# Optimization experiments

Hardware: AMD Instinct MI355X
Metric: run time of the kernel (lower is better)

The kernel has to match this reference:

```python
import jax, jax.numpy as jnp
import numpy as np

D_INPUT = 2048
DD_DIM = 512
DD_PAIRS = DD_DIM // 2


def setup_inputs() -> dict:
    key = jax.random.key(0)
    k1, k2, k3 = jax.random.split(key, 3)
    x = jax.random.normal(k1, (4, 4096, D_INPUT), dtype=jnp.float32)
    # Learned projection (zeros at init in torch; use small random for a non-trivial test)
    W = jax.random.normal(k2, (DD_PAIRS, D_INPUT), dtype=jnp.float32) * 0.02
    b = jax.random.normal(k3, (DD_PAIRS,), dtype=jnp.float32) * 0.02
    return {"x": x, "W": W, "b": b}


def reference(x, W, b):
    # x: (B, T, D); W: (P, D); b: (P,) with P = DD_DIM // 2
    deltas = jnp.einsum('btd,pd->btp', x, W) + b          # (B, T, P)
    angles = jnp.cumsum(deltas, axis=1)                   # cumulative phase
    cos, sin = jnp.cos(angles), jnp.sin(angles)
    x1 = x[..., :DD_PAIRS]                                # (B, T, P)
    x2 = x[..., DD_PAIRS:DD_DIM]                          # (B, T, P)
    rotated = jnp.concatenate([x1 * cos - x2 * sin, x2 * cos + x1 * sin], axis=-1)
    return jnp.concatenate([rotated, x[..., DD_DIM:]], axis=-1)
```

## Files before the change

### kernel.cpp

```cpp
#include <hip/hip_runtime.h>
#include <math.h>

#define BB 4
#define TT 4096
#define DDIM 2048
#define PP 256
#define MM (BB*TT)
#define KKDIM 2048
#define CHUNK 32
#define NCHUNK (TT/CHUNK)

#define BK 32
#define KSTEPS (KKDIM/BK)
#define LROW 72

typedef __attribute__((ext_vector_type(8))) short short8;
typedef __attribute__((ext_vector_type(4))) float f32x4;

__device__ __forceinline__ unsigned short f2bf(float f) {
    unsigned u = __float_as_uint(f);
    u += 0x7FFF + ((u >> 16) & 1);
    return (unsigned short)(u >> 16);
}
__device__ __forceinline__ float bf2f(unsigned short h) {
    return __uint_as_float(((unsigned)h) << 16);
}

__device__ __forceinline__ void cvt8(const float4& va, const float4& vb,
                                     short8& hi, short8& lo) {
    float f[8] = {va.x, va.y, va.z, va.w, vb.x, vb.y, vb.z, vb.w};
    #pragma unroll
    for (int j = 0; j < 8; ++j) {
        unsigned short h = f2bf(f[j]);
        hi[j] = (short)h;
        lo[j] = (short)f2bf(f[j] - bf2f(h));
    }
}

__device__ __forceinline__ void cvt4(const float4& v, uint2& hp, uint2& lp) {
    unsigned short h0 = f2bf(v.x), h1 = f2bf(v.y), h2 = f2bf(v.z), h3 = f2bf(v.w);
    unsigned short l0 = f2bf(v.x - bf2f(h0)), l1 = f2bf(v.y - bf2f(h1));
    unsigned short l2 = f2bf(v.z - bf2f(h2)), l3 = f2bf(v.w - bf2f(h3));
    hp.x = (unsigned)h0 | ((unsigned)h1 << 16); hp.y = (unsigned)h2 | ((unsigned)h3 << 16);
    lp.x = (unsigned)l0 | ((unsigned)l1 << 16); lp.y = (unsigned)l2 | ((unsigned)l3 << 16);
}

__global__ __launch_bounds__(256) void prep_wf_k(const float* __restrict__ W,
                                                 unsigned short* __restrict__ Wfh,
                                                 unsigned short* __restrict__ Wfl) {
    const int f = blockIdx.x * 256 + threadIdx.x;
    const int lane = f & 63;
    const int nb   = (f >> 6) & 15;
    const int k0i  = f >> 10;
    const int row  = nb * 16 + (lane & 15);
    const int kk   = k0i * 32 + (lane >> 4) * 8;
    const float* src = W + (size_t)row * KKDIM + kk;
    float4 a = *(const float4*)src;
    float4 b = *(const float4*)(src + 4);
    short8 hi, lo;
    cvt8(a, b, hi, lo);
    *(short8*)(Wfh + (size_t)f * 8) = hi;
    *(short8*)(Wfl + (size_t)f * 8) = lo;
}

#define GSTEP(CUR, NXT, BHc, BLc, BHn, BLn, IT)                               \
{                                                                             \
    const bool last_ = ((IT) == KSTEPS - 1);                                  \
    const int  kA_   = last_ ? (IT) * BK : ((IT) + 1) * BK;                   \
    float4 av0_ = *(const float4*)(xs0 + kA_);                                \
    float4 av1_ = *(const float4*)(xs1 + kA_);                                \
    const int k0iN_ = last_ ? (IT) : (IT) + 1;                                \
    _Pragma("unroll")                                                         \
    for (int nt = 0; nt < 2; ++nt) {                                          \
        size_t o = bfbase + (size_t)(k0iN_ * 16 + nt) * 512;                  \
        BHn[nt] = *(const short8*)(Wfh + o);                                  \
        BLn[nt] = *(const short8*)(Wfl + o);                                  \
    }                                                                         \
    short8 ah_[2], al_[2];                                                    \
    _Pragma("unroll")                                                         \
    for (int mt = 0; mt < 2; ++mt) {                                          \
        int idx = (wm * 32 + mt * 16 + lm) * LROW + ko * 8;                   \
        ah_[mt] = *(const short8*)&Ast[CUR][idx];                             \
        al_[mt] = *(const short8*)&Ast[CUR][idx + 32];                        \
    }                                                                         \
    _Pragma("unroll")                                                         \
    for (int mt = 0; mt < 2; ++mt)                                            \
        _Pragma("unroll")                                                     \
        for (int nt = 0; nt < 2; ++nt) {                                      \
            f32x4 c = acc[mt][nt];                                            \
            c = __builtin_amdgcn_mfma_f32_16x16x32_bf16(ah_[mt], BHc[nt], c, 0, 0, 0); \
            c = __builtin_amdgcn_mfma_f32_16x16x32_bf16(ah_[mt], BLc[nt], c, 0, 0, 0); \
            c = __builtin_amdgcn_mfma_f32_16x16x32_bf16(al_[mt], BHc[nt], c, 0, 0, 0); \
            acc[mt][nt] = c;                                                  \
        }                                                                     \
    uint2 hp0_, lp0_, hp1_, lp1_;                                             \
    cvt4(av0_, hp0_, lp0_);                                                   \
    cvt4(av1_, hp1_, lp1_);                                                   \
    *(uint2*)&Ast[NXT][sidx0]      = hp0_;                                    \
    *(uint2*)&Ast[NXT][sidx0 + 32] = lp0_;                                    \
    *(uint2*)&Ast[NXT][sidx1]      = hp1_;                                    \
    *(uint2*)&Ast[NXT][sidx1 + 32] = lp1_;                                    \
    if (docopy && !last_ && kA_ >= 512) {                                     \
        *(float4*)(os0 + kA_) = av0_;                                         \
        *(float4*)(os1 + kA_) = av1_;                                         \
    }                                                                         \
    __syncthreads();                                                          \
}

__global__ __launch_bounds__(512, 4) void gemm4_k(const float* __restrict__ x,
                                                  const unsigned short* __restrict__ Wfh,
                                                  const unsigned short* __restrict__ Wfl,
                                                  const float* __restrict__ bias,
                                                  float* __restrict__ delta,
                                                  float* __restrict__ csum,
                                                  float* __restrict__ out) {
    __shared__ unsigned short Ast[2][128 * LROW];

    const int hw      = blockIdx.y * 4 + blockIdx.x;
    const int logical = (hw & 7) * 64 + (hw >> 3);
    const int nidx    = logical & 3;
    const int midx    = logical >> 2;
    const int n0      = nidx * 64;
    const int m0      = midx * 128;
    const bool docopy = (nidx == 0);

    const int tid  = threadIdx.x;
    const int w    = tid >> 6;
    const int wm   = w >> 1;
    const int wn   = w & 1;
    const int lane = tid & 63;
    const int lm   = lane & 15;
    const int ko   = lane >> 4;

    const int arow0 = tid >> 3;
    const int ach   = tid & 7;
    const int sidx0 = arow0 * LROW + ach * 4;
    const int sidx1 = (64 + arow0) * LROW + ach * 4;
    const float* xs0 = x + (size_t)(m0 + arow0) * KKDIM + ach * 4;
    const float* xs1 = x + (size_t)(m0 + 64 + arow0) * KKDIM + ach * 4;
    float* os0 = out + (size_t)(m0 + arow0) * DDIM + ach * 4;
    float* os1 = out + (size_t)(m0 + 64 + arow0) * DDIM + ach * 4;

    const size_t bfbase = ((size_t)(nidx * 4 + wn * 2) * 64 + (size_t)lane) * 8;

    f32x4 acc[2][2];
    #pragma unroll
    for (int i = 0; i < 2; ++i)
        #pragma unroll
        for (int j = 0; j < 2; ++j) {
            f32x4 z = {0.f, 0.f, 0.f, 0.f};
            acc[i][j] = z;
        }

    short8 bhA[2], blA[2], bhB[2], blB[2];

    {
        float4 a0 = *(const float4*)(xs0);
        float4 a1 = *(const float4*)(xs1);
        uint2 hp, lp;
        cvt4(a0, hp, lp);
        *(uint2*)&Ast[0][sidx0]      = hp;
        *(uint2*)&Ast[0][sidx0 + 32] = lp;
        cvt4(a1, hp, lp);
        *(uint2*)&Ast[0][sidx1]      = hp;
        *(uint2*)&Ast[0][sidx1 + 32] = lp;
        #pragma unroll
        for (int nt = 0; nt < 2; ++nt) {
            size_t o = bfbase + (size_t)nt * 512;
            bhA[nt] = *(const short8*)(Wfh + o);
            blA[nt] = *(const short8*)(Wfl + o);
        }
        __syncthreads();
    }

    for (int it = 0; it < KSTEPS; it += 2) {
        GSTEP(0, 1, bhA, blA, bhB, blB, it)
        GSTEP(1, 0, bhB, blB, bhA, blA, it + 1)
    }

    float bsv[2];
    #pragma unroll
    for (int nt = 0; nt < 2; ++nt) bsv[nt] = bias[n0 + wn * 32 + nt * 16 + lm];

    float cs[2] = {0.f, 0.f};
    #pragma unroll
    for (int mt = 0; mt < 2; ++mt)
        #pragma unroll
        for (int nt = 0; nt < 2; ++nt)
            #pragma unroll
            for (int r = 0; r < 4; ++r) {
                float val = acc[mt][nt][r] + bsv[nt];
                int m = m0 + wm * 32 + mt * 16 + ko * 4 + r;
                delta[(size_t)m * PP + n0 + wn * 32 + nt * 16 + lm] = val;
                cs[nt] += val;
            }
    #pragma unroll
    for (int nt = 0; nt < 2; ++nt) {
        float s = cs[nt];
        s += __shfl_xor(s, 16);
        s += __shfl_xor(s, 32);
        if (lane < 16)
            csum[(size_t)(m0 / CHUNK + wm) * PP + n0 + wn * 32 + nt * 16 + lane] = s;
    }
}

__global__ __launch_bounds__(256) void rotate4_k(const float* __restrict__ delta,
                                                 const float* __restrict__ csum,
                                                 const float* __restrict__ x,
                                                 float* __restrict__ out) {
    const int blk = blockIdx.x;
    const int seg = blk & 3;
    const int bc  = blk >> 2;
    const int c   = bc & (NCHUNK - 1);
    const int b   = bc >> 7;
    const int p   = threadIdx.x;

    const float* cs = csum + (size_t)(b * NCHUNK) * PP + p;
    float angle = 0.f;
    int c0 = 0;
    for (; c0 + 16 <= c; c0 += 16) {
        float v[16];
        #pragma unroll
        for (int j = 0; j < 16; ++j) v[j] = cs[(size_t)(c0 + j) * PP];
        #pragma unroll
        for (int j = 0; j < 16; ++j) angle += v[j];
    }
    for (; c0 < c; ++c0) angle += cs[(size_t)c0 * PP];

    const int tbase = bc * CHUNK;
    const float* dp = delta + (size_t)tbase * PP + p;

    const int tpre = seg * 8;
    for (int t = 0; t < tpre; t += 8) {
        float v[8];
        #pragma unroll
        for (int j = 0; j < 8; ++j) v[j] = dp[(size_t)(t + j) * PP];
        #pragma unroll
        for (int j = 0; j < 8; ++j) angle += v[j];
    }

    const float* xp = x + (size_t)tbase * DDIM + p;
    float*       op = out + (size_t)tbase * DDIM + p;
    const float inv2pi = 0.15915494309189535f;

    for (int t0 = tpre; t0 < tpre + 8; t0 += 4) {
        float dv[4], x1v[4], x2v[4];
        #pragma unroll
        for (int j = 0; j < 4; ++j) {
            dv[j]  = dp[(size_t)(t0 + j) * PP];
            x1v[j] = xp[(size_t)(t0 + j) * DDIM];
            x2v[j] = xp[(size_t)(t0 + j) * DDIM + PP];
        }
        #pragma unroll
        for (int j = 0; j < 4; ++j) {
            angle += dv[j];
            float r  = __builtin_amdgcn_fractf(angle * inv2pi);
            float s  = __builtin_amdgcn_sinf(r);
            float co = __builtin_amdgcn_cosf(r);
            op[(size_t)(t0 + j) * DDIM]      = x1v[j] * co - x2v[j] * s;
            op[(size_t)(t0 + j) * DDIM + PP] = x2v[j] * co + x1v[j] * s;
        }
    }
}

__global__ __launch_bounds__(256) void gemm_k(const float* __restrict__ x,
                                              const float* __restrict__ W,
                                              const float* __restrict__ bias,
                                              float* __restrict__ delta,
                                              int dstride, int doff) {
    __shared__ float As[16][68];
    __shared__ float Bs[16][68];
    const int m0  = blockIdx.x * 64;
    const int n0  = blockIdx.y * 64;
    const int tid = threadIdx.x;
    const int lr  = tid >> 2;
    const int lc  = (tid & 3) << 2;
    const int tmi = tid & 15;
    const int tni = tid >> 4;
    float acc[4][4] = {};
    for (int k0 = 0; k0 < KKDIM; k0 += 16) {
        float4 a4 = *(const float4*)(x + (size_t)(m0 + lr) * KKDIM + k0 + lc);
        float4 b4 = *(const float4*)(W + (size_t)(n0 + lr) * KKDIM + k0 + lc);
        __syncthreads();
        As[lc + 0][lr] = a4.x; As[lc + 1][lr] = a4.y;
        As[lc + 2][lr] = a4.z; As[lc + 3][lr] = a4.w;
        Bs[lc + 0][lr] = b4.x; Bs[lc + 1][lr] = b4.y;
        Bs[lc + 2][lr] = b4.z; Bs[lc + 3][lr] = b4.w;
        __syncthreads();
        #pragma unroll
        for (int kk = 0; kk < 16; ++kk) {
            float4 av = *(const float4*)&As[kk][tmi * 4];
            float4 bv = *(const float4*)&Bs[kk][tni * 4];
            float am[4] = {av.x, av.y, av.z, av.w};
            float bn[4] = {bv.x, bv.y, bv.z, bv.w};
            #pragma unroll
            for (int i = 0; i < 4; ++i)
                #pragma unroll
                for (int j = 0; j < 4; ++j)
                    acc[i][j] += am[i] * bn[j];
        }
    }
    const float4 b4 = *(const float4*)(bias + n0 + tni * 4);
    #pragma unroll
    for (int i = 0; i < 4; ++i) {
        size_t m = (size_t)(m0 + tmi * 4 + i);
        float4 o;
        o.x = acc[i][0] + b4.x; o.y = acc[i][1] + b4.y;
        o.z = acc[i][2] + b4.z; o.w = acc[i][3] + b4.w;
        *(float4*)(delta + m * dstride + doff + n0 + tni * 4) = o;
    }
}

__global__ __launch_bounds__(256) void chunksum_k(const float* __restrict__ delta,
                                                  int dstride, int doff,
                                                  float* __restrict__ csum, int cstride) {
    const int bc = blockIdx.x;
    const int b  = bc / NCHUNK;
    const int c  = bc % NCHUNK;
    const int p  = threadIdx.x;
    const int tbase = b * TT + c * CHUNK;
    float s = 0.f;
    #pragma unroll 8
    for (int t = 0; t < CHUNK; ++t)
        s += delta[(size_t)(tbase + t) * dstride + doff + p];
    csum[(size_t)bc * cstride + p] = s;
}

__global__ __launch_bounds__(256) void scan_k(float* __restrict__ csum, int cstride) {
    const int idx = blockIdx.x * 256 + threadIdx.x;
    const int b = idx >> 8;
    const int p = idx & 255;
    float run = 0.f;
    for (int c0 = 0; c0 < NCHUNK; c0 += 8) {
        float v[8];
        #pragma unroll
        for (int j = 0; j < 8; ++j)
            v[j] = csum[(size_t)(b * NCHUNK + c0 + j) * cstride + p];
        #pragma unroll
        for (int j = 0; j < 8; ++j) {
            float t = v[j];
            csum[(size_t)(b * NCHUNK + c0 + j) * cstride + p] = run;
            run += t;
        }
    }
}

__global__ __launch_bounds__(256) void rotate_k(const float* __restrict__ delta,
                                                int dstride, int doff,
                                                const float* __restrict__ csum, int cstride,
                                                const float* __restrict__ x,
                                                float* __restrict__ out) {
    const int bc = blockIdx.x;
    const int p  = threadIdx.x;
    const int tbase = bc * CHUNK;
    float angle = csum[(size_t)bc * cstride + p];
    for (int t = 0; t < CHUNK; ++t) {
        size_t row = (size_t)(tbase + t);
        angle += delta[row * dstride + doff + p];
        float s, co;
        sincosf(angle, &s, &co);
        float x1 = x[row * DDIM + p];
        float x2 = x[row * DDIM + PP + p];
        out[row * DDIM + p]      = x1 * co - x2 * s;
        out[row * DDIM + PP + p] = x2 * co + x1 * s;
    }
}

__global__ __launch_bounds__(256) void copy_k(const float* __restrict__ x,
                                              float* __restrict__ out) {
    const size_t row = (size_t)blockIdx.x * 4 + (threadIdx.x >> 6);
    const int lane = threadIdx.x & 63;
    const int col = 512 + (blockIdx.y * 64 + lane) * 4;
    const size_t a = row * DDIM + col;
    *(float4*)(out + a) = *(const float4*)(x + a);
}

extern "C" void kernel_launch(void* const* d_in, const int* in_sizes, int n_in,
                              void* d_out, int out_size, void* d_ws, size_t ws_size,
                              hipStream_t stream) {
    const float* x    = (const float*)d_in[0];
    const float* W    = (const float*)d_in[1];
    const float* bias = (const float*)d_in[2];
    float* out = (float*)d_out;

    const size_t delta_elems = (size_t)MM * PP;
    const size_t csum_elems  = (size_t)BB * NCHUNK * PP;
    const size_t w_elems     = (size_t)PP * KKDIM;
    const size_t need = (delta_elems + csum_elems) * sizeof(float)
                      + 2 * w_elems * sizeof(unsigned short);

    if (ws_size >= need) {
        float* delta = (float*)d_ws;
        float* csum  = (float*)d_ws + delta_elems;
        unsigned short* Wfh = (unsigned short*)(csum + csum_elems);
        unsigned short* Wfl = Wfh + w_elems;
        prep_wf_k<<<256, 256, 0, stream>>>(W, Wfh, Wfl);
        gemm4_k<<<dim3(4, MM / 128), 512, 0, stream>>>(x, Wfh, Wfl, bias,
                                                       delta, csum, out);
        rotate4_k<<<BB * NCHUNK * 4, 256, 0, stream>>>(delta, csum, x, out);
    } else {
        float* delta = out; const int dstride = DDIM, doff = 512;
        float* csum  = out + 768; const int cstride = DDIM;
        gemm_k<<<dim3(MM / 64, PP / 64), 256, 0, stream>>>(x, W, bias, delta, dstride, doff);
        chunksum_k<<<BB * NCHUNK, 256, 0, stream>>>(delta, dstride, doff, csum, cstride);
        scan_k<<<(BB * PP) / 256, 256, 0, stream>>>(csum, cstride);
        rotate_k<<<BB * NCHUNK, 256, 0, stream>>>(delta, dstride, doff, csum, cstride, x, out);
        copy_k<<<dim3(MM / 4, 6), 256, 0, stream>>>(x, out);
    }
}
```

Measured before the change: 316.1 us.

## Deepen x prefetch to two stages and use a lightweight LDS-only barrier

```diff
diff --git a/kernel.cpp b/kernel.cpp
--- a/kernel.cpp
+++ b/kernel.cpp
@@ -63,51 +63,69 @@
     *(short8*)(Wfl + (size_t)f * 8) = lo;
 }
 
-#define GSTEP(CUR, NXT, BHc, BLc, BHn, BLn, IT)                               \
-{                                                                             \
-    const bool last_ = ((IT) == KSTEPS - 1);                                  \
-    const int  kA_   = last_ ? (IT) * BK : ((IT) + 1) * BK;                   \
-    float4 av0_ = *(const float4*)(xs0 + kA_);                                \
-    float4 av1_ = *(const float4*)(xs1 + kA_);                                \
-    const int k0iN_ = last_ ? (IT) : (IT) + 1;                                \
-    _Pragma("unroll")                                                         \
-    for (int nt = 0; nt < 2; ++nt) {                                          \
-        size_t o = bfbase + (size_t)(k0iN_ * 16 + nt) * 512;                  \
-        BHn[nt] = *(const short8*)(Wfh + o);                                  \
-        BLn[nt] = *(const short8*)(Wfl + o);                                  \
-    }                                                                         \
-    short8 ah_[2], al_[2];                                                    \
-    _Pragma("unroll")                                                         \
-    for (int mt = 0; mt < 2; ++mt) {                                          \
-        int idx = (wm * 32 + mt * 16 + lm) * LROW + ko * 8;                   \
-        ah_[mt] = *(const short8*)&Ast[CUR][idx];                             \
-        al_[mt] = *(const short8*)&Ast[CUR][idx + 32];                        \
-    }                                                                         \
-    _Pragma("unroll")                                                         \
-    for (int mt = 0; mt < 2; ++mt)                                            \
-        _Pragma("unroll")                                                     \
-        for (int nt = 0; nt < 2; ++nt) {                                      \
-            f32x4 c = acc[mt][nt];                                            \
+#define GBAR()                                                                 \
+    do {                                                                       \
+        asm volatile("s_waitcnt lgkmcnt(0)" ::: "memory");                     \
+        __builtin_amdgcn_sched_barrier(0);                                     \
+        __builtin_amdgcn_s_barrier();                                          \
+        __builtin_amdgcn_sched_barrier(0);                                     \
+    } while (0)
+
+#define GSTEP(CUR, NXT, BHc, BLc, BHn, BLn, ANa0, ANa1, AFa0, AFa1, IT)        \
+{                                                                              \
+    const int itN_ = (IT) + 1;                                                 \
+    const int itF_ = ((IT) + 2 < KSTEPS) ? (IT) + 2 : KSTEPS - 1;              \
+                \
+    AFa0 = *(const float4*)(xs0 + itF_ * BK);                                  \
+    AFa1 = *(const float4*)(xs1 + itF_ * BK);                                  \
+                                              \
+    const int k0iN_ = (itN_ < KSTEPS) ? itN_ : KSTEPS - 1;                     \
+    _Pragma("unroll")                                                          \
+    for (int nt = 0; nt < 2; ++nt) {                                           \
+        size_t o = bfbase + (size_t)(k0iN_ * 16 + nt) * 512;                   \
+        BHn[nt] = *(const short8*)(Wfh + o);                                   \
+        BLn[nt] = *(const short8*)(Wfl + o);                                   \
+    }                                                                          \
+       \
+    {                                                                          \
+        uint2 hp_, lp_;                                                        \
+        cvt4(ANa0, hp_, lp_);                                                  \
+        *(uint2*)&Ast[NXT][sidx0]      = hp_;                                  \
+        *(uint2*)&Ast[NXT][sidx0 + 32] = lp_;                                  \
+        cvt4(ANa1, hp_, lp_);                                                  \
+        *(uint2*)&Ast[NXT][sidx1]      = hp_;                                  \
+        *(uint2*)&Ast[NXT][sidx1 + 32] = lp_;                                  \
+    }                                                                          \
+                                    \
+    if (docopy && itN_ < KSTEPS) {                                             \
+        const int kN_ = itN_ * BK;                                             \
+        if (kN_ >= 512) {                                                      \
+            *(float4*)(os0 + kN_) = ANa0;                                      \
+            *(float4*)(os1 + kN_) = ANa1;                                      \
+        }                                                                      \
+    }                                                                          \
+                                     \
+    short8 ah_[2], al_[2];                                                     \
+    _Pragma("unroll")                                                          \
+    for (int mt = 0; mt < 2; ++mt) {                                           \
+        int idx = (wm * 32 + mt * 16 + lm) * LROW + ko * 8;                    \
+        ah_[mt] = *(const short8*)&Ast[CUR][idx];                              \
+        al_[mt] = *(const short8*)&Ast[CUR][idx + 32];                         \
+    }                                                                          \
+    _Pragma("unroll")                                                          \
+    for (int mt = 0; mt < 2; ++mt)                                             \
+        _Pragma("unroll")                                                      \
+        for (int nt = 0; nt < 2; ++nt) {                                       \
+            f32x4 c = acc[mt][nt];                                             \
             c = __builtin_amdgcn_mfma_f32_16x16x32_bf16(ah_[mt], BHc[nt], c, 0, 0, 0); \
             c = __builtin_amdgcn_mfma_f32_16x16x32_bf16(ah_[mt], BLc[nt], c, 0, 0, 0); \
             c = __builtin_amdgcn_mfma_f32_16x16x32_bf16(al_[mt], BHc[nt], c, 0, 0, 0); \
-            acc[mt][nt] = c;                                                  \
-        }                                                                     \
-    uint2 hp0_, lp0_, hp1_, lp1_;                                             \
-    cvt4(av0_, hp0_, lp0_);                                                   \
-    cvt4(av1_, hp1_, lp1_);                                                   \
-    *(uint2*)&Ast[NXT][sidx0]      = hp0_;                                    \
-    *(uint2*)&Ast[NXT][sidx0 + 32] = lp0_;                                    \
-    *(uint2*)&Ast[NXT][sidx1]      = hp1_;                                    \
-    *(uint2*)&Ast[NXT][sidx1 + 32] = lp1_;                                    \
-    if (docopy && !last_ && kA_ >= 512) {                                     \
-        *(float4*)(os0 + kA_) = av0_;                                         \
-        *(float4*)(os1 + kA_) = av1_;                                         \
-    }                                                                         \
-    __syncthreads();                                                          \
-}
-
-__global__ __launch_bounds__(512, 4) void gemm4_k(const float* __restrict__ x,
+            acc[mt][nt] = c;                                                   \
+        }                                                                      \
+    GBAR();                                                                    \
+}
+
+__global__ __launch_bounds__(512, 4) void gemm5_k(const float* __restrict__ x,
                                                   const unsigned short* __restrict__ Wfh,
                                                   const unsigned short* __restrict__ Wfl,
                                                   const float* __restrict__ bias,
@@ -152,30 +170,33 @@
             acc[i][j] = z;
         }
 
+    float4 aA0, aA1, aB0, aB1;
     short8 bhA[2], blA[2], bhB[2], blB[2];
 
     {
-        float4 a0 = *(const float4*)(xs0);
-        float4 a1 = *(const float4*)(xs1);
-        uint2 hp, lp;
-        cvt4(a0, hp, lp);
-        *(uint2*)&Ast[0][sidx0]      = hp;
-        *(uint2*)&Ast[0][sidx0 + 32] = lp;
-        cvt4(a1, hp, lp);
-        *(uint2*)&Ast[0][sidx1]      = hp;
-        *(uint2*)&Ast[0][sidx1 + 32] = lp;
+        float4 p0 = *(const float4*)(xs0);
+        float4 p1 = *(const float4*)(xs1);
+        aA0 = *(const float4*)(xs0 + BK);
+        aA1 = *(const float4*)(xs1 + BK);
         #pragma unroll
         for (int nt = 0; nt < 2; ++nt) {
             size_t o = bfbase + (size_t)nt * 512;
             bhA[nt] = *(const short8*)(Wfh + o);
             blA[nt] = *(const short8*)(Wfl + o);
         }
-        __syncthreads();
+        uint2 hp, lp;
+        cvt4(p0, hp, lp);
+        *(uint2*)&Ast[0][sidx0]      = hp;
+        *(uint2*)&Ast[0][sidx0 + 32] = lp;
+        cvt4(p1, hp, lp);
+        *(uint2*)&Ast[0][sidx1]      = hp;
+        *(uint2*)&Ast[0][sidx1 + 32] = lp;
+        GBAR();
     }
 
     for (int it = 0; it < KSTEPS; it += 2) {
-        GSTEP(0, 1, bhA, blA, bhB, blB, it)
-        GSTEP(1, 0, bhB, blB, bhA, blA, it + 1)
+        GSTEP(0, 1, bhA, blA, bhB, blB, aA0, aA1, aB0, aB1, it)
+        GSTEP(1, 0, bhB, blB, bhA, blA, aB0, aB1, aA0, aA1, it + 1)
     }
 
     float bsv[2];
@@ -395,7 +416,7 @@
         unsigned short* Wfh = (unsigned short*)(csum + csum_elems);
         unsigned short* Wfl = Wfh + w_elems;
         prep_wf_k<<<256, 256, 0, stream>>>(W, Wfh, Wfl);
-        gemm4_k<<<dim3(4, MM / 128), 512, 0, stream>>>(x, Wfh, Wfl, bias,
+        gemm5_k<<<dim3(4, MM / 128), 512, 0, stream>>>(x, Wfh, Wfl, bias,
                                                        delta, csum, out);
         rotate4_k<<<BB * NCHUNK * 4, 256, 0, stream>>>(delta, csum, x, out);
     } else {
```

Result: slower. 325.5 us (+3.0%).
